# Optimization experiments

Measured on AMD Instinct MI355X. Metric: run time of the kernel, lower is better.

The kernel has to match this reference:

```python
import jax, jax.numpy as jnp
import numpy as np
from jax import lax


def _box_conv3d(x, win):
    k = jnp.ones((1, 1, win, win, win), x.dtype) / float(win ** 3)
    pad = win // 2
    return lax.conv_general_dilated(
        x, k,
        window_strides=(1, 1, 1),
        padding=[(pad, pad)] * 3,
        dimension_numbers=('NCDHW', 'OIDHW', 'NCDHW'),
    )


def setup_inputs() -> dict:
    key = jax.random.key(0)
    k1, k2 = jax.random.split(key)
    shape = (1, 1, 160, 192, 224)
    pred = jax.random.uniform(k1, shape, dtype=jnp.float32)
    target = jax.random.uniform(k2, shape, dtype=jnp.float32)
    return {'pred': pred, 'target': target, 'window_size': 9}


def reference(pred, target, window_size):
    Ii = target
    Ji = pred
    win = window_size
    mu1 = _box_conv3d(Ii, win)
    mu2 = _box_conv3d(Ji, win)
    mu1_sq = mu1 * mu1
    mu2_sq = mu2 * mu2
    mu1_mu2 = mu1 * mu2
    sigma1_sq = _box_conv3d(Ii * Ii, win) - mu1_sq
    sigma2_sq = _box_conv3d(Ji * Ji, win) - mu2_sq
    sigma12 = _box_conv3d(Ii * Ji, win) - mu1_mu2
    eps = jnp.finfo(sigma12.dtype).eps
    cc = sigma12 * sigma12 / jnp.maximum(sigma1_sq * sigma2_sq, eps)
    return -jnp.mean(cc)
```

## Files before the change

kernel.cpp:

```cpp
#include <hip/hip_runtime.h>
#include <hip/hip_fp16.h>

#define D_  160
#define H_  192
#define W_  224
#define HW_ (H_ * W_)
#define HW2_ (HW_ / 2)
#define N_  (D_ * H_ * W_)
#define INV729 (1.0f / 729.0f)
#define HSEG 16
#define NSEG (H_ / HSEG)
#define NSTEP2 13

__device__ __forceinline__ int PI4(int i) { return i + ((i >> 5) << 2); }


__global__ void k_init(double* acc) { *acc = 0.0; }

__device__ __forceinline__ unsigned pack2(float a, float b) {
    const __half2 h = __floats2half2_rn(a, b);
    return *(const unsigned*)&h;
}

__global__ __launch_bounds__(128) void k_passWH(const float* __restrict__ pred,
                                                const float* __restrict__ targ,
                                                uint4* __restrict__ outA,
                                                unsigned* __restrict__ outB) {
    __shared__ __attribute__((aligned(16))) float bI[2][2][264];
    __shared__ __attribute__((aligned(16))) float bJ[2][2][264];
    const int d  = blockIdx.x;
    const int h0 = blockIdx.y * HSEG;
    const int t  = threadIdx.x;
    const long dbase = (long)d * HW_;

    const bool stg = (t < 116);
    const int  sa  = (t >= 58) ? 1 : 0;
    const int  sc  = sa ? (t - 58) : t;
    const bool interior = (sc >= 1) && (sc <= 56);
    const float* src = sa ? pred : targ;
    const long srcoff = dbase + (long)(4 * sc - 4);

    const bool cmp = (t < 112);
    const int  l   = t;

    float2 q[5][9];
    #pragma unroll
    for (int c = 0; c < 5; ++c)
        #pragma unroll
        for (int k = 0; k < 9; ++k) q[c][k] = make_float2(0.f, 0.f);
    float S0[5] = {0,0,0,0,0}, S1[5] = {0,0,0,0,0};

    float4 pf0 = make_float4(0.f,0.f,0.f,0.f), pf1 = pf0;
    auto fetch = [&](int p, float4& f) {
        f = make_float4(0.f, 0.f, 0.f, 0.f);
        const int hh = h0 - 5 + p;
        if (stg && interior && p < 26 && hh >= 0 && hh < H_)
            f = *(const float4*)(src + srcoff + (long)hh * W_);
    };
    fetch(0, pf0);
    fetch(1, pf1);

    #pragma unroll
    for (int k = 0; k < NSTEP2; ++k) {
        const int cur = k & 1;
        if (stg) {
            float* base = sa ? &bJ[cur][0][0] : &bI[cur][0][0];
            const int p0 = PI4(4 * sc);
            *(float4*)(base + p0)       = pf0;
            *(float4*)(base + 264 + p0) = pf1;
        }
        fetch(2 * k + 2, pf0);
        fetch(2 * k + 3, pf1);
        __syncthreads();

        if (cmp) {
            #pragma unroll
            for (int r = 0; r < 2; ++r) {
                const int p = 2 * k + r;
                float a[10], b[10];
                #pragma unroll
                for (int m = 0; m < 5; ++m) {
                    const int pp = PI4(2 * l + 2 * m);
                    a[2*m] = bI[cur][r][pp]; a[2*m+1] = bI[cur][r][pp + 1];
                    b[2*m] = bJ[cur][r][pp]; b[2*m+1] = bJ[cur][r][pp + 1];
                }
                float sI = 0.f, sJ = 0.f, sII = 0.f, sJJ = 0.f, sIJ = 0.f;
                #pragma unroll
                for (int kk = 0; kk < 9; ++kk) {
                    sI  += a[kk];          sJ  += b[kk];
                    sII += a[kk] * a[kk];  sJJ += b[kk] * b[kk];
                    sIJ += a[kk] * b[kk];
                }
                float w0[5], w1[5];
                w0[0] = sI;  w1[0] = sI  + a[9] - a[0];
                w0[1] = sJ;  w1[1] = sJ  + b[9] - b[0];
                w0[2] = sII; w1[2] = sII + a[9]*a[9] - a[0]*a[0];
                w0[3] = sJJ; w1[3] = sJJ + b[9]*b[9] - b[0]*b[0];
                w0[4] = sIJ; w1[4] = sIJ + a[9]*b[9] - a[0]*b[0];

                const int ph = p % 9;
                #pragma unroll
                for (int c = 0; c < 5; ++c) {
                    S0[c] += w0[c] - q[c][ph].x;
                    S1[c] += w1[c] - q[c][ph].y;
                    q[c][ph].x = w0[c];
                    q[c][ph].y = w1[c];
                }
                if (p >= 9 && (p - 9) < HSEG) {
                    const long rb = dbase + (long)(h0 + p - 9) * W_;
                    uint4 oA;
                    oA.x = pack2(S0[0], S0[1]); oA.y = pack2(S0[2], S0[3]);
                    oA.z = pack2(S1[0], S1[1]); oA.w = pack2(S1[2], S1[3]);
                    outA[rb / 2 + l] = oA;
                    outB[rb / 2 + l] = pack2(S0[4], S1[4]);
                }
            }
        }
    }
}

__global__ __launch_bounds__(256) void k_passD(const uint4* __restrict__ bufA,
                                               const unsigned* __restrict__ bufB,
                                               double* __restrict__ acc) {
    const int DSEG = D_ / 8;
    const int p2 = blockIdx.x * blockDim.x + threadIdx.x;
    const int d0 = blockIdx.y * DSEG;

    float2 q[5][9], S[5];
    #pragma unroll
    for (int c = 0; c < 5; ++c) S[c] = make_float2(0.f, 0.f);

    #pragma unroll
    for (int k = 0; k < 9; ++k) {
        const int dd = d0 - 5 + k;
        uint4 va = make_uint4(0u, 0u, 0u, 0u);
        unsigned vb = 0u;
        if (dd >= 0) {
            va = bufA[(long)dd * HW2_ + p2];
            vb = bufB[(long)dd * HW2_ + p2];
        }
        const float2 a01 = __half22float2(*(const __half2*)&va.x);
        const float2 a23 = __half22float2(*(const __half2*)&va.y);
        const float2 b01 = __half22float2(*(const __half2*)&va.z);
        const float2 b23 = __half22float2(*(const __half2*)&va.w);
        const float2 c44 = __half22float2(*(const __half2*)&vb);
        q[0][k] = make_float2(a01.x, b01.x); S[0].x += a01.x; S[0].y += b01.x;
        q[1][k] = make_float2(a01.y, b01.y); S[1].x += a01.y; S[1].y += b01.y;
        q[2][k] = make_float2(a23.x, b23.x); S[2].x += a23.x; S[2].y += b23.x;
        q[3][k] = make_float2(a23.y, b23.y); S[3].x += a23.y; S[3].y += b23.y;
        q[4][k] = make_float2(c44.x, c44.y); S[4].x += c44.x; S[4].y += c44.y;
    }

    float myacc = 0.f;
    #pragma unroll
    for (int j = 0; j < DSEG; ++j) {
        const int dd = d0 + 4 + j;
        uint4 va = make_uint4(0u, 0u, 0u, 0u);
        unsigned vb = 0u;
        if (dd < D_) {
            va = bufA[(long)dd * HW2_ + p2];
            vb = bufB[(long)dd * HW2_ + p2];
        }
        const float2 a01 = __half22float2(*(const __half2*)&va.x);
        const float2 a23 = __half22float2(*(const __half2*)&va.y);
        const float2 b01 = __half22float2(*(const __half2*)&va.z);
        const float2 b23 = __half22float2(*(const __half2*)&va.w);
        const float2 c44 = __half22float2(*(const __half2*)&vb);
        const float2 nv[5] = {
            make_float2(a01.x, b01.x), make_float2(a01.y, b01.y),
            make_float2(a23.x, b23.x), make_float2(a23.y, b23.y),
            make_float2(c44.x, c44.y)
        };
        const int ph = j % 9;
        #pragma unroll
        for (int c = 0; c < 5; ++c) {
            S[c].x += nv[c].x - q[c][ph].x;
            S[c].y += nv[c].y - q[c][ph].y;
            q[c][ph] = nv[c];
        }
        #pragma unroll
        for (int e = 0; e < 2; ++e) {
            const float mu1 = (e ? S[0].y : S[0].x) * INV729;
            const float mu2 = (e ? S[1].y : S[1].x) * INV729;
            const float s1  = (e ? S[2].y : S[2].x) * INV729 - mu1 * mu1;
            const float s2  = (e ? S[3].y : S[3].x) * INV729 - mu2 * mu2;
            const float s12 = (e ? S[4].y : S[4].x) * INV729 - mu1 * mu2;
            const float den = fmaxf(s1 * s2, 1.1920929e-7f);
            myacc += (s12 * s12) / den;
        }
    }

    __shared__ float red[256];
    red[threadIdx.x] = myacc;
    __syncthreads();
    #pragma unroll
    for (int s = 128; s > 0; s >>= 1) {
        if (threadIdx.x < s) red[threadIdx.x] += red[threadIdx.x + s];
        __syncthreads();
    }
    if (threadIdx.x == 0) atomicAdd(acc, (double)red[0]);
}

__global__ void k_fin(const double* __restrict__ acc, float* __restrict__ out) {
    out[0] = (float)(-(*acc) / (double)N_);
}

extern "C" void kernel_launch(void* const* d_in, const int* in_sizes, int n_in,
                              void* d_out, int out_size, void* d_ws, size_t ws_size,
                              hipStream_t stream) {
    const float* pred = (const float*)d_in[0];
    const float* targ = (const float*)d_in[1];

    uint4*    bufA = (uint4*)d_ws;
    unsigned* bufB = (unsigned*)((char*)d_ws + (size_t)(N_ / 2) * 16);
    double*   acc  = (double*)((char*)d_ws + (size_t)(N_ / 2) * 16 + (size_t)(N_ / 2) * 4);
    float*    out  = (float*)d_out;

    k_init<<<1, 1, 0, stream>>>(acc);
    dim3 g1(D_, NSEG);
    k_passWH<<<g1, 128, 0, stream>>>(pred, targ, bufA, bufB);
    dim3 g3(HW2_ / 256, 8);
    k_passD<<<g3, 256, 0, stream>>>(bufA, bufB, acc);
    k_fin<<<1, 1, 0, stream>>>(acc, out);
}
```

Baseline: 64.79 us.

## Replace LDS staging in W/H pass with wavefront shuffles and per-wave half-row units

The W/H box-sum pass no longer stages rows through shared memory with double buffering and block barriers. Each 64-lane wavefront now handles half a row width over a 24-row H segment, loads float2 directly from global memory with a one-row register prefetch, and builds the 9-wide W window with __shfl_down. This removes the __syncthreads and LDS traffic and raises HSEG, which cuts the H halo overhead. The cost is narrower float2 loads, halo columns loaded twice across the two halves, and shuffle instructions in place of LDS reads.

New measurement: 73.28 us. 13.1% more time.

```diff
diff --git a/kernel.cpp b/kernel.cpp
--- a/kernel.cpp
+++ b/kernel.cpp
@@ -8,11 +8,10 @@
 #define HW2_ (HW_ / 2)
 #define N_  (D_ * H_ * W_)
 #define INV729 (1.0f / 729.0f)
-#define HSEG 16
+#define HSEG 24
 #define NSEG (H_ / HSEG)
-#define NSTEP2 13
-
-__device__ __forceinline__ int PI4(int i) { return i + ((i >> 5) << 2); }
+#define NROW (HSEG + 9)
+#define UPD  (NSEG * 2)
 
 
 __global__ void k_init(double* acc) { *acc = 0.0; }
@@ -22,26 +21,24 @@
     return *(const unsigned*)&h;
 }
 
-__global__ __launch_bounds__(128) void k_passWH(const float* __restrict__ pred,
+__global__ __launch_bounds__(256) void k_passWH(const float* __restrict__ pred,
                                                 const float* __restrict__ targ,
                                                 uint4* __restrict__ outA,
                                                 unsigned* __restrict__ outB) {
-    __shared__ __attribute__((aligned(16))) float bI[2][2][264];
-    __shared__ __attribute__((aligned(16))) float bJ[2][2][264];
-    const int d  = blockIdx.x;
-    const int h0 = blockIdx.y * HSEG;
-    const int t  = threadIdx.x;
+    const int unit = blockIdx.x * 4 + (threadIdx.x >> 6);
+    const int lane = threadIdx.x & 63;
+    const int d    = unit / UPD;
+    const int rem  = unit % UPD;
+    const int half = rem & 1;
+    const int h0   = (rem >> 1) * HSEG;
     const long dbase = (long)d * HW_;
-
-    const bool stg = (t < 116);
-    const int  sa  = (t >= 58) ? 1 : 0;
-    const int  sc  = sa ? (t - 58) : t;
-    const bool interior = (sc >= 1) && (sc <= 56);
-    const float* src = sa ? pred : targ;
-    const long srcoff = dbase + (long)(4 * sc - 4);
-
-    const bool cmp = (t < 112);
-    const int  l   = t;
+    const int wbase = half * 112;
+
+    const int  wld  = wbase - 4 + 2 * lane;
+    const bool ldok = (lane < 60) && (wld >= 0) && (wld + 1 < W_);
+    const float* pI = targ + dbase + wld;
+    const float* pJ = pred + dbase + wld;
+    const bool cmp = (lane < 56);
 
     float2 q[5][9];
     #pragma unroll
@@ -50,72 +47,67 @@
         for (int k = 0; k < 9; ++k) q[c][k] = make_float2(0.f, 0.f);
     float S0[5] = {0,0,0,0,0}, S1[5] = {0,0,0,0,0};
 
-    float4 pf0 = make_float4(0.f,0.f,0.f,0.f), pf1 = pf0;
-    auto fetch = [&](int p, float4& f) {
-        f = make_float4(0.f, 0.f, 0.f, 0.f);
-        const int hh = h0 - 5 + p;
-        if (stg && interior && p < 26 && hh >= 0 && hh < H_)
-            f = *(const float4*)(src + srcoff + (long)hh * W_);
-    };
-    fetch(0, pf0);
-    fetch(1, pf1);
-
-    #pragma unroll
-    for (int k = 0; k < NSTEP2; ++k) {
-        const int cur = k & 1;
-        if (stg) {
-            float* base = sa ? &bJ[cur][0][0] : &bI[cur][0][0];
-            const int p0 = PI4(4 * sc);
-            *(float4*)(base + p0)       = pf0;
-            *(float4*)(base + 264 + p0) = pf1;
-        }
-        fetch(2 * k + 2, pf0);
-        fetch(2 * k + 3, pf1);
-        __syncthreads();
-
-        if (cmp) {
-            #pragma unroll
-            for (int r = 0; r < 2; ++r) {
-                const int p = 2 * k + r;
-                float a[10], b[10];
-                #pragma unroll
-                for (int m = 0; m < 5; ++m) {
-                    const int pp = PI4(2 * l + 2 * m);
-                    a[2*m] = bI[cur][r][pp]; a[2*m+1] = bI[cur][r][pp + 1];
-                    b[2*m] = bJ[cur][r][pp]; b[2*m+1] = bJ[cur][r][pp + 1];
-                }
-                float sI = 0.f, sJ = 0.f, sII = 0.f, sJJ = 0.f, sIJ = 0.f;
-                #pragma unroll
-                for (int kk = 0; kk < 9; ++kk) {
-                    sI  += a[kk];          sJ  += b[kk];
-                    sII += a[kk] * a[kk];  sJJ += b[kk] * b[kk];
-                    sIJ += a[kk] * b[kk];
-                }
-                float w0[5], w1[5];
-                w0[0] = sI;  w1[0] = sI  + a[9] - a[0];
-                w0[1] = sJ;  w1[1] = sJ  + b[9] - b[0];
-                w0[2] = sII; w1[2] = sII + a[9]*a[9] - a[0]*a[0];
-                w0[3] = sJJ; w1[3] = sJJ + b[9]*b[9] - b[0]*b[0];
-                w0[4] = sIJ; w1[4] = sIJ + a[9]*b[9] - a[0]*b[0];
-
-                const int ph = p % 9;
-                #pragma unroll
-                for (int c = 0; c < 5; ++c) {
-                    S0[c] += w0[c] - q[c][ph].x;
-                    S1[c] += w1[c] - q[c][ph].y;
-                    q[c][ph].x = w0[c];
-                    q[c][ph].y = w1[c];
-                }
-                if (p >= 9 && (p - 9) < HSEG) {
-                    const long rb = dbase + (long)(h0 + p - 9) * W_;
-                    uint4 oA;
-                    oA.x = pack2(S0[0], S0[1]); oA.y = pack2(S0[2], S0[3]);
-                    oA.z = pack2(S1[0], S1[1]); oA.w = pack2(S1[2], S1[3]);
-                    outA[rb / 2 + l] = oA;
-                    outB[rb / 2 + l] = pack2(S0[4], S1[4]);
-                }
+    float2 cI = make_float2(0.f, 0.f), cJ = cI, nI, nJ;
+    {
+        const int hh = h0 - 5;
+        if (ldok && hh >= 0) {
+            cI = *(const float2*)(pI + (long)hh * W_);
+            cJ = *(const float2*)(pJ + (long)hh * W_);
+        }
+    }
+
+    #pragma unroll
+    for (int p = 0; p < NROW; ++p) {
+        nI = make_float2(0.f, 0.f); nJ = nI;
+        {
+            const int hh = h0 - 4 + p;
+            if (ldok && (p + 1 < NROW) && hh >= 0 && hh < H_) {
+                nI = *(const float2*)(pI + (long)hh * W_);
+                nJ = *(const float2*)(pJ + (long)hh * W_);
             }
         }
+
+        float a[10], b[10];
+        a[0] = cI.x; a[1] = cI.y; b[0] = cJ.x; b[1] = cJ.y;
+        #pragma unroll
+        for (int j = 1; j <= 4; ++j) {
+            a[2*j]   = __shfl_down(cI.x, j);
+            a[2*j+1] = __shfl_down(cI.y, j);
+            b[2*j]   = __shfl_down(cJ.x, j);
+            b[2*j+1] = __shfl_down(cJ.y, j);
+        }
+
+        float sI = 0.f, sJ = 0.f, sII = 0.f, sJJ = 0.f, sIJ = 0.f;
+        #pragma unroll
+        for (int kk = 0; kk < 9; ++kk) {
+            sI  += a[kk];          sJ  += b[kk];
+            sII += a[kk] * a[kk];  sJJ += b[kk] * b[kk];
+            sIJ += a[kk] * b[kk];
+        }
+        float w0[5], w1[5];
+        w0[0] = sI;  w1[0] = sI  + a[9] - a[0];
+        w0[1] = sJ;  w1[1] = sJ  + b[9] - b[0];
+        w0[2] = sII; w1[2] = sII + a[9]*a[9] - a[0]*a[0];
+        w0[3] = sJJ; w1[3] = sJJ + b[9]*b[9] - b[0]*b[0];
+        w0[4] = sIJ; w1[4] = sIJ + a[9]*b[9] - a[0]*b[0];
+
+        const int ph = p % 9;
+        #pragma unroll
+        for (int c = 0; c < 5; ++c) {
+            S0[c] += w0[c] - q[c][ph].x;
+            S1[c] += w1[c] - q[c][ph].y;
+            q[c][ph].x = w0[c];
+            q[c][ph].y = w1[c];
+        }
+        if (p >= 9 && cmp) {
+            const long rb = dbase + (long)(h0 + p - 9) * W_;
+            uint4 oA;
+            oA.x = pack2(S0[0], S0[1]); oA.y = pack2(S0[2], S0[3]);
+            oA.z = pack2(S1[0], S1[1]); oA.w = pack2(S1[2], S1[3]);
+            outA[rb / 2 + half * 56 + lane] = oA;
+            outB[rb / 2 + half * 56 + lane] = pack2(S0[4], S1[4]);
+        }
+        cI = nI; cJ = nJ;
     }
 }
 
@@ -217,8 +209,7 @@
     float*    out  = (float*)d_out;
 
     k_init<<<1, 1, 0, stream>>>(acc);
-    dim3 g1(D_, NSEG);
-    k_passWH<<<g1, 128, 0, stream>>>(pred, targ, bufA, bufB);
+    k_passWH<<<D_ * UPD / 4, 256, 0, stream>>>(pred, targ, bufA, bufB);
     dim3 g3(HW2_ / 256, 8);
     k_passD<<<g3, 256, 0, stream>>>(bufA, bufB, acc);
     k_fin<<<1, 1, 0, stream>>>(acc, out);
```
